# Kernel optimization log

Hardware: AMD Instinct MI355X
Metric: run time of the kernel (lower is better)

Reference implementation:

```python
import jax, jax.numpy as jnp
import numpy as np

WP = 1.0     # warp_penalty
TEMP = 0.01  # soft-min temperature
BIG = 1e7    # finite stand-in for +inf (exp(-BIG/TEMP) == 0 exactly in fp32)


def setup_inputs() -> dict:
    key = jax.random.key(0)
    k1, k2, k3, k4 = jax.random.split(key, 4)
    B, T1, T2, C = 8, 256, 1024, 128
    fea_a = jax.random.normal(k1, (B, T1, C), jnp.float32)
    fea_b = jax.random.normal(k2, (B, T2, C), jnp.float32)
    len_a = jax.random.randint(k3, (B,), T1 // 2, T1 + 1)
    len_b = jax.random.randint(k4, (B,), T2 // 2, T2 + 1)
    return {"fea_a": fea_a, "len_a": len_a, "fea_b": fea_b, "len_b": len_b}


def _softmin(v, temp):
    # v: [3, B, T1]; stable -temp*log(sum(exp(-v/temp)))
    m = jnp.min(v, axis=0)
    return m - temp * jnp.log(jnp.sum(jnp.exp(-(v - m) / temp), axis=0))


def _soft_dtw(fea_a, fea_b, len_a, len_b, wp=WP, temp=TEMP):
    B, T1, C = fea_a.shape
    T2 = fea_b.shape[1]
    # L1 cost: [B, T2, T1]  (rows index fea_b, cols index fea_a, as in torch code)
    cost = jnp.mean(jnp.abs(fea_a[:, None, :, :] - fea_b[:, :, None, :]), axis=-1)
    # skewed cost: skew[b, d, j] = cost[b, clip(d-j, 0, T2-1), j]
    D = T1 + T2 - 1
    d = jnp.arange(D)[:, None]
    j = jnp.arange(T1)[None, :]
    idx = jnp.clip(d - j, 0, T2 - 1)           # [D, T1]
    skew = cost[:, idx, j]                      # [B, D, T1]
    skew = jnp.swapaxes(skew, 0, 1)             # [D, B, T1] for scan

    pc0 = jnp.full((B, T1 + 1), BIG, jnp.float32)       # path_cost (diag d-1)
    pcp0 = pc0.at[:, 0].set(0.0)                         # path_cost_prev (diag d-2)

    def step(carry, crow):
        pc, pcp = carry
        dirs = jnp.stack([pcp[:, :-1], pc[:, 1:] + wp, pc[:, :-1] + wp], axis=0)
        new = crow + _softmin(dirs, temp)                # [B, T1]
        new = jnp.concatenate([jnp.full((B, 1), BIG, new.dtype), new], axis=1)
        return (new, pc), new

    _, ys = jax.lax.scan(step, (pc0, pcp0), skew)        # ys: [D, B, T1+1]
    # per-sample answer: diagonal len_a+len_b-2, entry len_a
    di = len_a + len_b - 2
    loss_i = ys[di, jnp.arange(B), len_a]
    return jnp.sum(loss_i)  # reduction='mean' over a length-1 accumulator == sum


def reference(fea_a, len_a, fea_b, len_b):
    return _soft_dtw(fea_a, fea_b, len_a, len_b)
```

## Files before the change

### kernel.cpp

```cpp
#include <hip/hip_runtime.h>
#include <hip/hip_bf16.h>
#include <cstddef>

#define BIGV 10000000.0f
#define WPV  1.0f

#define BATCH 8
#define T1N 256
#define T2N 1024
#define CN 128
#define DN 1279

#define RPB 16
#define NSLOT 3
#define SLOT_BYTES (RPB * 1024)

__global__ __launch_bounds__(256) void cost_kernel(const float* __restrict__ A,
                                                   const float* __restrict__ Bf,
                                                   const int* __restrict__ lenA,
                                                   const int* __restrict__ lenB,
                                                   float* __restrict__ sk) {
    __shared__ float As[64 * 64];
    __shared__ float Bs[127 * 64];

    const int b  = blockIdx.z;
    const int d0 = blockIdx.y * 64;
    const int j0 = blockIdx.x * 64;
    const int tid = threadIdx.x;

    const int dEnd = lenA[b] + lenB[b] - 2;
    if (d0 > dEnd) return;

    const float* Ab = A  + (size_t)b * T1N * CN;
    const float* Bb = Bf + (size_t)b * T2N * CN;

    const int tj = tid & 15;
    const int td = tid >> 4;
    const int brow0 = td - tj + 63;
    const int rbase = d0 - j0 - 63;

    float acc[4][4];
    #pragma unroll
    for (int i = 0; i < 4; ++i)
        #pragma unroll
        for (int j = 0; j < 4; ++j) acc[i][j] = 0.0f;

#define SW(row, cq) (((row) << 6) + ((((cq) + (row)) & 15) << 2))

    for (int h = 0; h < 2; ++h) {
        const int ch0 = h * 64;
        #pragma unroll
        for (int i = 0; i < 4; ++i) {
            int idx = tid + i * 256;
            int row = idx >> 4;
            int cq  = idx & 15;
            float4 f = *(const float4*)(Ab + (size_t)(j0 + row) * CN + ch0 + (cq << 2));
            *(float4*)&As[SW(row, cq)] = f;
        }
        #pragma unroll
        for (int i = 0; i < 8; ++i) {
            int idx = tid + i * 256;
            if (idx < 2032) {
                int row = idx >> 4;
                int cq  = idx & 15;
                int gr = rbase + row;
                gr = gr < 0 ? 0 : (gr > T2N - 1 ? T2N - 1 : gr);
                float4 f = *(const float4*)(Bb + (size_t)gr * CN + ch0 + (cq << 2));
                *(float4*)&Bs[SW(row, cq)] = f;
            }
        }
        __syncthreads();

        for (int cq = 0; cq < 16; ++cq) {
            float4 a4[4], bv[7];
            #pragma unroll
            for (int ji = 0; ji < 4; ++ji) {
                int row = tj + 16 * ji;
                a4[ji] = *(const float4*)&As[SW(row, cq)];
            }
            #pragma unroll
            for (int m = 0; m < 7; ++m) {
                int row = brow0 + 16 * (m - 3);
                bv[m] = *(const float4*)&Bs[SW(row, cq)];
            }
            #pragma unroll
            for (int dk = 0; dk < 4; ++dk) {
                #pragma unroll
                for (int ji = 0; ji < 4; ++ji) {
                    float4 aa = a4[ji];
                    float4 bb = bv[dk - ji + 3];
                    acc[dk][ji] += fabsf(aa.x - bb.x) + fabsf(aa.y - bb.y)
                                 + fabsf(aa.z - bb.z) + fabsf(aa.w - bb.w);
                }
            }
        }
        __syncthreads();
    }
#undef SW

    #pragma unroll
    for (int dk = 0; dk < 4; ++dk) {
        int d = d0 + td + 16 * dk;
        if (d < DN) {
            size_t rowoff = ((size_t)b * DN + d) * T1N;
            #pragma unroll
            for (int ji = 0; ji < 4; ++ji) {
                int j = j0 + tj + 16 * ji;
                sk[rowoff + j] = acc[dk][ji] * (1.0f / 128.0f);
            }
        }
    }
}

__global__ __launch_bounds__(128, 1) void dp_wave_kernel(const float* __restrict__ sk,
                                                         const int* __restrict__ lenA,
                                                         const int* __restrict__ lenB,
                                                         float* __restrict__ out) {
    __shared__ char ring[NSLOT * SLOT_BYTES];
    __shared__ int prod_cnt;
    __shared__ int cons_cnt;

    const int b = blockIdx.x;
    if (threadIdx.x == 0) { prod_cnt = 0; cons_cnt = 0; }
    __syncthreads();

    const int wave = threadIdx.x >> 6;
    const int L = threadIdx.x & 63;

    const int la = __builtin_amdgcn_readfirstlane(lenA[b]);
    const int lb = __builtin_amdgcn_readfirstlane(lenB[b]);
    const int dEnd = la + lb - 2;
    const int kLast = dEnd >> 4;
    const int nblk = kLast + 1;

    if (wave == 1) {
        const float* skbp = sk + (size_t)b * DN * T1N + (L << 2);
        for (int k = 0; k < nblk; ++k) {
            if (k >= NSLOT) {
                while (__hip_atomic_load(&cons_cnt, __ATOMIC_ACQUIRE,
                                         __HIP_MEMORY_SCOPE_WORKGROUP) < k - (NSLOT - 1))
                    __builtin_amdgcn_s_sleep(1);
            }
            char* slot = ring + (k % NSLOT) * SLOT_BYTES;
            const int r0 = k * RPB;
            #pragma unroll
            for (int r = 0; r < RPB; ++r) {
                int row = r0 + r; row = row > DN - 1 ? DN - 1 : row;
                __builtin_amdgcn_global_load_lds(
                    (const __attribute__((address_space(1))) void*)(skbp + (size_t)row * T1N),
                    (__attribute__((address_space(3))) void*)(slot + (r << 10)),
                    16, 0, 0);
            }
            asm volatile("s_waitcnt vmcnt(16)" ::: "memory");
            if (L == 0)
                __hip_atomic_store(&prod_cnt, k, __ATOMIC_RELEASE,
                                   __HIP_MEMORY_SCOPE_WORKGROUP);
        }
        asm volatile("s_waitcnt vmcnt(0)" ::: "memory");
        if (L == 0)
            __hip_atomic_store(&prod_cnt, nblk, __ATOMIC_RELEASE,
                               __HIP_MEMORY_SCOPE_WORKGROUP);
        return;
    }

    float v1_0 = BIGV, v1_1 = BIGV, v1_2 = BIGV, v1_3 = BIGV;
    float v2_0 = BIGV, v2_1 = BIGV, v2_2 = BIGV, v2_3 = BIGV;
    float p1_prev = (L == 0) ? 0.0f : BIGV;

#define SHFL_UP1(SRC)                                                       \
    __int_as_float(__builtin_amdgcn_update_dpp(                             \
        __float_as_int(BIGV), __float_as_int(SRC),                          \
        0x138 , 0xF, 0xF, false))

#define DP_STEP(C4) do {                                                    \
        float4 c = (C4);                                                    \
        float p1 = SHFL_UP1(v1_3);                                          \
        float p2 = p1_prev;                                                 \
        float n0 = c.x + fminf(p2,   fminf(v1_0, p1)   + WPV);              \
        float n1 = c.y + fminf(v2_0, fminf(v1_1, v1_0) + WPV);              \
        float n2 = c.z + fminf(v2_1, fminf(v1_2, v1_1) + WPV);              \
        float n3 = c.w + fminf(v2_2, fminf(v1_3, v1_2) + WPV);              \
        p1_prev = p1;                                                       \
        v2_0 = v1_0; v2_1 = v1_1; v2_2 = v1_2; v2_3 = v1_3;                 \
        v1_0 = n0;   v1_1 = n1;   v1_2 = n2;   v1_3 = n3;                   \
    } while (0)

#define DP_STEP_G(C4, R) do {                                               \
        float4 c = (C4);                                                    \
        float p1 = SHFL_UP1(v1_3);                                          \
        float p2 = p1_prev;                                                 \
        float n0 = c.x + fminf(p2,   fminf(v1_0, p1)   + WPV);              \
        float n1 = c.y + fminf(v2_0, fminf(v1_1, v1_0) + WPV);              \
        float n2 = c.z + fminf(v2_1, fminf(v1_2, v1_1) + WPV);              \
        float n3 = c.w + fminf(v2_2, fminf(v1_3, v1_2) + WPV);              \
        if ((R) <= rem) {                                                   \
            p1_prev = p1;                                                   \
            v2_0 = v1_0; v2_1 = v1_1; v2_2 = v1_2; v2_3 = v1_3;             \
            v1_0 = n0;   v1_1 = n1;   v1_2 = n2;   v1_3 = n3;               \
        }                                                                   \
    } while (0)

#define WAIT_BLK(K) do {                                                    \
        while (__hip_atomic_load(&prod_cnt, __ATOMIC_ACQUIRE,               \
                                 __HIP_MEMORY_SCOPE_WORKGROUP) < (K) + 1)   \
            __builtin_amdgcn_s_sleep(1);                                    \
    } while (0)

#define READ_BLK(K)                                                         \
        const char* slot = ring + ((K) % NSLOT) * SLOT_BYTES;               \
        const float4* rp = (const float4*)(slot + (L << 4));                \
        float4 c0  = rp[0 * 64],  c1  = rp[1 * 64],  c2  = rp[2 * 64],  c3  = rp[3 * 64];  \
        float4 c4_ = rp[4 * 64],  c5  = rp[5 * 64],  c6  = rp[6 * 64],  c7  = rp[7 * 64];  \
        float4 c8  = rp[8 * 64],  c9  = rp[9 * 64],  c10 = rp[10 * 64], c11 = rp[11 * 64]; \
        float4 c12 = rp[12 * 64], c13 = rp[13 * 64], c14 = rp[14 * 64], c15 = rp[15 * 64]; \
        __builtin_amdgcn_sched_barrier(0);

    for (int k = 0; k < kLast; ++k) {
        WAIT_BLK(k);
        READ_BLK(k);
        DP_STEP(c0);  DP_STEP(c1);  DP_STEP(c2);  DP_STEP(c3);
        DP_STEP(c4_); DP_STEP(c5);  DP_STEP(c6);  DP_STEP(c7);
        DP_STEP(c8);  DP_STEP(c9);  DP_STEP(c10); DP_STEP(c11);
        DP_STEP(c12); DP_STEP(c13); DP_STEP(c14); DP_STEP(c15);
        if (L == 0)
            __hip_atomic_store(&cons_cnt, k + 1, __ATOMIC_RELEASE,
                               __HIP_MEMORY_SCOPE_WORKGROUP);
    }

    {
        const int rem = dEnd & 15;
        WAIT_BLK(kLast);
        READ_BLK(kLast);
        DP_STEP_G(c0, 0);   DP_STEP_G(c1, 1);   DP_STEP_G(c2, 2);   DP_STEP_G(c3, 3);
        DP_STEP_G(c4_, 4);  DP_STEP_G(c5, 5);   DP_STEP_G(c6, 6);   DP_STEP_G(c7, 7);
        DP_STEP_G(c8, 8);   DP_STEP_G(c9, 9);   DP_STEP_G(c10, 10); DP_STEP_G(c11, 11);
        DP_STEP_G(c12, 12); DP_STEP_G(c13, 13); DP_STEP_G(c14, 14); DP_STEP_G(c15, 15);
    }

    const int tcap = la - 1;
    if (L == (tcap >> 2)) {
        const int k = tcap & 3;
        float r = v1_0;
        if (k == 1) r = v1_1;
        else if (k == 2) r = v1_2;
        else if (k == 3) r = v1_3;
        atomicAdd(out, r);
    }
#undef READ_BLK
#undef WAIT_BLK
#undef DP_STEP_G
#undef DP_STEP
#undef SHFL_UP1
}

extern "C" void kernel_launch(void* const* d_in, const int* in_sizes, int n_in,
                              void* d_out, int out_size, void* d_ws, size_t ws_size,
                              hipStream_t stream) {
    const float* feaA = (const float*)d_in[0];
    const int*   lenA = (const int*)d_in[1];
    const float* feaB = (const float*)d_in[2];
    const int*   lenB = (const int*)d_in[3];

    float* sk = (float*)d_ws;

    hipMemsetAsync(d_out, 0, sizeof(float), stream);
    cost_kernel<<<dim3(T1N / 64, (DN + 63) / 64, BATCH), 256, 0, stream>>>(feaA, feaB, lenA, lenB, sk);
    dp_wave_kernel<<<BATCH, 128, 0, stream>>>(sk, lenA, lenB, (float*)d_out);
}
```

Baseline: 160.3 us.

## Replace producer-wave ring with single-wave self-prefetched LDS pipeline

Removes the dedicated producer wave and the LDS atomic counters it used to hand blocks to the consumer. The DP wave now issues its own async global-to-LDS loads three blocks ahead into a four-slot ring and waits on vmcnt instead of spin-polling shared counters. This drops the sleep/poll handshake latency from the serial critical path, but the DMA issue now sits inside the consumer's loop. Correctness depends on in-order vmcnt accounting and on no slot being overwritten while it is still being read.

```diff
diff --git a/kernel.cpp b/kernel.cpp
--- a/kernel.cpp
+++ b/kernel.cpp
@@ -12,7 +12,7 @@
 #define DN 1279
 
 #define RPB 16
-#define NSLOT 3
+#define NSLOT 4
 #define SLOT_BYTES (RPB * 1024)
 
 __global__ __launch_bounds__(256) void cost_kernel(const float* __restrict__ A,
@@ -112,56 +112,34 @@
     }
 }
 
-__global__ __launch_bounds__(128, 1) void dp_wave_kernel(const float* __restrict__ sk,
-                                                         const int* __restrict__ lenA,
-                                                         const int* __restrict__ lenB,
-                                                         float* __restrict__ out) {
+__global__ __launch_bounds__(64, 1) void dp_wave_kernel(const float* __restrict__ sk,
+                                                        const int* __restrict__ lenA,
+                                                        const int* __restrict__ lenB,
+                                                        float* __restrict__ out) {
     __shared__ char ring[NSLOT * SLOT_BYTES];
-    __shared__ int prod_cnt;
-    __shared__ int cons_cnt;
 
     const int b = blockIdx.x;
-    if (threadIdx.x == 0) { prod_cnt = 0; cons_cnt = 0; }
-    __syncthreads();
-
-    const int wave = threadIdx.x >> 6;
-    const int L = threadIdx.x & 63;
+    const int L = threadIdx.x;
 
     const int la = __builtin_amdgcn_readfirstlane(lenA[b]);
     const int lb = __builtin_amdgcn_readfirstlane(lenB[b]);
     const int dEnd = la + lb - 2;
     const int kLast = dEnd >> 4;
-    const int nblk = kLast + 1;
-
-    if (wave == 1) {
-        const float* skbp = sk + (size_t)b * DN * T1N + (L << 2);
-        for (int k = 0; k < nblk; ++k) {
-            if (k >= NSLOT) {
-                while (__hip_atomic_load(&cons_cnt, __ATOMIC_ACQUIRE,
-                                         __HIP_MEMORY_SCOPE_WORKGROUP) < k - (NSLOT - 1))
-                    __builtin_amdgcn_s_sleep(1);
-            }
-            char* slot = ring + (k % NSLOT) * SLOT_BYTES;
-            const int r0 = k * RPB;
-            #pragma unroll
-            for (int r = 0; r < RPB; ++r) {
-                int row = r0 + r; row = row > DN - 1 ? DN - 1 : row;
-                __builtin_amdgcn_global_load_lds(
-                    (const __attribute__((address_space(1))) void*)(skbp + (size_t)row * T1N),
-                    (__attribute__((address_space(3))) void*)(slot + (r << 10)),
-                    16, 0, 0);
-            }
-            asm volatile("s_waitcnt vmcnt(16)" ::: "memory");
-            if (L == 0)
-                __hip_atomic_store(&prod_cnt, k, __ATOMIC_RELEASE,
-                                   __HIP_MEMORY_SCOPE_WORKGROUP);
-        }
-        asm volatile("s_waitcnt vmcnt(0)" ::: "memory");
-        if (L == 0)
-            __hip_atomic_store(&prod_cnt, nblk, __ATOMIC_RELEASE,
-                               __HIP_MEMORY_SCOPE_WORKGROUP);
-        return;
-    }
+
+    const float* skbp = sk + (size_t)b * DN * T1N + (L << 2);
+
+#define DMA_BLK(K) do {                                                     \
+        char* _slot = ring + ((K) & (NSLOT - 1)) * SLOT_BYTES;              \
+        const int _r0 = (K) * RPB;                                          \
+        _Pragma("unroll")                                                   \
+        for (int _r = 0; _r < RPB; ++_r) {                                  \
+            int _row = _r0 + _r; _row = _row > DN - 1 ? DN - 1 : _row;      \
+            __builtin_amdgcn_global_load_lds(                               \
+                (const __attribute__((address_space(1))) void*)(skbp + (size_t)_row * T1N), \
+                (__attribute__((address_space(3))) void*)(_slot + (_r << 10)), \
+                16, 0, 0);                                                  \
+        }                                                                   \
+    } while (0)
 
     float v1_0 = BIGV, v1_1 = BIGV, v1_2 = BIGV, v1_3 = BIGV;
     float v2_0 = BIGV, v2_1 = BIGV, v2_2 = BIGV, v2_3 = BIGV;
@@ -200,14 +178,10 @@
         }                                                                   \
     } while (0)
 
-#define WAIT_BLK(K) do {                                                    \
-        while (__hip_atomic_load(&prod_cnt, __ATOMIC_ACQUIRE,               \
-                                 __HIP_MEMORY_SCOPE_WORKGROUP) < (K) + 1)   \
-            __builtin_amdgcn_s_sleep(1);                                    \
-    } while (0)
+#define WAIT32() asm volatile("s_waitcnt vmcnt(32)" ::: "memory")
 
 #define READ_BLK(K)                                                         \
-        const char* slot = ring + ((K) % NSLOT) * SLOT_BYTES;               \
+        const char* slot = ring + ((K) & (NSLOT - 1)) * SLOT_BYTES;         \
         const float4* rp = (const float4*)(slot + (L << 4));                \
         float4 c0  = rp[0 * 64],  c1  = rp[1 * 64],  c2  = rp[2 * 64],  c3  = rp[3 * 64];  \
         float4 c4_ = rp[4 * 64],  c5  = rp[5 * 64],  c6  = rp[6 * 64],  c7  = rp[7 * 64];  \
@@ -215,27 +189,29 @@
         float4 c12 = rp[12 * 64], c13 = rp[13 * 64], c14 = rp[14 * 64], c15 = rp[15 * 64]; \
         __builtin_amdgcn_sched_barrier(0);
 
+    DMA_BLK(0); DMA_BLK(1); DMA_BLK(2);
+
     for (int k = 0; k < kLast; ++k) {
-        WAIT_BLK(k);
+        WAIT32();
         READ_BLK(k);
+        DMA_BLK(k + 3);
         DP_STEP(c0);  DP_STEP(c1);  DP_STEP(c2);  DP_STEP(c3);
         DP_STEP(c4_); DP_STEP(c5);  DP_STEP(c6);  DP_STEP(c7);
         DP_STEP(c8);  DP_STEP(c9);  DP_STEP(c10); DP_STEP(c11);
         DP_STEP(c12); DP_STEP(c13); DP_STEP(c14); DP_STEP(c15);
-        if (L == 0)
-            __hip_atomic_store(&cons_cnt, k + 1, __ATOMIC_RELEASE,
-                               __HIP_MEMORY_SCOPE_WORKGROUP);
     }
 
     {
         const int rem = dEnd & 15;
-        WAIT_BLK(kLast);
+        WAIT32();
         READ_BLK(kLast);
         DP_STEP_G(c0, 0);   DP_STEP_G(c1, 1);   DP_STEP_G(c2, 2);   DP_STEP_G(c3, 3);
         DP_STEP_G(c4_, 4);  DP_STEP_G(c5, 5);   DP_STEP_G(c6, 6);   DP_STEP_G(c7, 7);
         DP_STEP_G(c8, 8);   DP_STEP_G(c9, 9);   DP_STEP_G(c10, 10); DP_STEP_G(c11, 11);
         DP_STEP_G(c12, 12); DP_STEP_G(c13, 13); DP_STEP_G(c14, 14); DP_STEP_G(c15, 15);
     }
+
+    asm volatile("s_waitcnt vmcnt(0)" ::: "memory");
 
     const int tcap = la - 1;
     if (L == (tcap >> 2)) {
@@ -247,10 +223,11 @@
         atomicAdd(out, r);
     }
 #undef READ_BLK
-#undef WAIT_BLK
+#undef WAIT32
 #undef DP_STEP_G
 #undef DP_STEP
 #undef SHFL_UP1
+#undef DMA_BLK
 }
 
 extern "C" void kernel_launch(void* const* d_in, const int* in_sizes, int n_in,
@@ -265,5 +242,5 @@
 
     hipMemsetAsync(d_out, 0, sizeof(float), stream);
     cost_kernel<<<dim3(T1N / 64, (DN + 63) / 64, BATCH), 256, 0, stream>>>(feaA, feaB, lenA, lenB, sk);
-    dp_wave_kernel<<<BATCH, 128, 0, stream>>>(sk, lenA, lenB, (float*)d_out);
+    dp_wave_kernel<<<BATCH, 64, 0, stream>>>(sk, lenA, lenB, (float*)d_out);
 }
```

Result: slower. 189.4 us (+18.2%).

## Fuse cost and DP kernels into one persistent launch with tile-ready counters

Applied to the files above, without the earlier changes.

Merges the cost-matrix kernel and the wavefront DP kernel into a single launch. Eight blocks run the DP while 256 worker blocks compute cost tiles in diagonal-major order and bump per-(batch, diagonal-band) global counters. The DP producer wave polls these counters before streaming rows, so the DP can start before the whole cost matrix exists. Wave priorities are also raised for the DP waves. The risks are correctness depending on the DP blocks and workers being co-resident, extra memset and atomic traffic, and DP blocks stalling on slow tiles.

```diff
diff --git a/kernel.cpp b/kernel.cpp
--- a/kernel.cpp
+++ b/kernel.cpp
@@ -10,122 +10,145 @@
 #define T2N 1024
 #define CN 128
 #define DN 1279
+#define NDT 20
+#define NTILE 640
+#define NWORK 256
 
 #define RPB 16
 #define NSLOT 3
 #define SLOT_BYTES (RPB * 1024)
-
-__global__ __launch_bounds__(256) void cost_kernel(const float* __restrict__ A,
-                                                   const float* __restrict__ Bf,
-                                                   const int* __restrict__ lenA,
-                                                   const int* __restrict__ lenB,
-                                                   float* __restrict__ sk) {
-    __shared__ float As[64 * 64];
-    __shared__ float Bs[127 * 64];
-
-    const int b  = blockIdx.z;
-    const int d0 = blockIdx.y * 64;
-    const int j0 = blockIdx.x * 64;
-    const int tid = threadIdx.x;
-
-    const int dEnd = lenA[b] + lenB[b] - 2;
-    if (d0 > dEnd) return;
-
-    const float* Ab = A  + (size_t)b * T1N * CN;
-    const float* Bb = Bf + (size_t)b * T2N * CN;
-
-    const int tj = tid & 15;
-    const int td = tid >> 4;
-    const int brow0 = td - tj + 63;
-    const int rbase = d0 - j0 - 63;
-
-    float acc[4][4];
-    #pragma unroll
-    for (int i = 0; i < 4; ++i)
-        #pragma unroll
-        for (int j = 0; j < 4; ++j) acc[i][j] = 0.0f;
+#define LDS_BYTES 49216
+
+__global__ __launch_bounds__(256, 1) void fused_kernel(const float* __restrict__ A,
+                                                       const float* __restrict__ Bf,
+                                                       const int* __restrict__ lenA,
+                                                       const int* __restrict__ lenB,
+                                                       float* __restrict__ sk,
+                                                       int* __restrict__ cnt,
+                                                       float* __restrict__ out) {
+    __shared__ __align__(16) char lds[LDS_BYTES];
+
+    const int bid = blockIdx.x;
+
+    if (bid >= BATCH) {
+        float* As = (float*)lds;
+        float* Bs = (float*)(lds + 16384);
+        const int tid = threadIdx.x;
+        const int tj = tid & 15;
+        const int td = tid >> 4;
 
 #define SW(row, cq) (((row) << 6) + ((((cq) + (row)) & 15) << 2))
 
-    for (int h = 0; h < 2; ++h) {
-        const int ch0 = h * 64;
-        #pragma unroll
-        for (int i = 0; i < 4; ++i) {
-            int idx = tid + i * 256;
-            int row = idx >> 4;
-            int cq  = idx & 15;
-            float4 f = *(const float4*)(Ab + (size_t)(j0 + row) * CN + ch0 + (cq << 2));
-            *(float4*)&As[SW(row, cq)] = f;
-        }
-        #pragma unroll
-        for (int i = 0; i < 8; ++i) {
-            int idx = tid + i * 256;
-            if (idx < 2032) {
-                int row = idx >> 4;
-                int cq  = idx & 15;
-                int gr = rbase + row;
-                gr = gr < 0 ? 0 : (gr > T2N - 1 ? T2N - 1 : gr);
-                float4 f = *(const float4*)(Bb + (size_t)gr * CN + ch0 + (cq << 2));
-                *(float4*)&Bs[SW(row, cq)] = f;
-            }
-        }
-        __syncthreads();
-
-        for (int cq = 0; cq < 16; ++cq) {
-            float4 a4[4], bv[7];
+        for (int t = bid - BATCH; t < NTILE; t += NWORK) {
+            const int y  = t >> 5;
+            const int b  = (t >> 2) & 7;
+            const int jb = t & 3;
+            const int d0 = y * 64;
+            const int j0 = jb * 64;
+
+            const int dEnd = lenA[b] + lenB[b] - 2;
+            if (d0 > dEnd) {
+                if (tid == 0)
+                    __hip_atomic_fetch_add(&cnt[b * NDT + y], 1,
+                                           __ATOMIC_RELEASE, __HIP_MEMORY_SCOPE_AGENT);
+                continue;
+            }
+
+            const float* Ab = A  + (size_t)b * T1N * CN;
+            const float* Bb = Bf + (size_t)b * T2N * CN;
+            const int brow0 = td - tj + 63;
+            const int rbase = d0 - j0 - 63;
+
+            float acc[4][4];
             #pragma unroll
-            for (int ji = 0; ji < 4; ++ji) {
-                int row = tj + 16 * ji;
-                a4[ji] = *(const float4*)&As[SW(row, cq)];
-            }
-            #pragma unroll
-            for (int m = 0; m < 7; ++m) {
-                int row = brow0 + 16 * (m - 3);
-                bv[m] = *(const float4*)&Bs[SW(row, cq)];
-            }
+            for (int i = 0; i < 4; ++i)
+                #pragma unroll
+                for (int j = 0; j < 4; ++j) acc[i][j] = 0.0f;
+
+            for (int h = 0; h < 2; ++h) {
+                const int ch0 = h * 64;
+                #pragma unroll
+                for (int i = 0; i < 4; ++i) {
+                    int idx = tid + i * 256;
+                    int row = idx >> 4;
+                    int cq  = idx & 15;
+                    float4 f = *(const float4*)(Ab + (size_t)(j0 + row) * CN + ch0 + (cq << 2));
+                    *(float4*)&As[SW(row, cq)] = f;
+                }
+                #pragma unroll
+                for (int i = 0; i < 8; ++i) {
+                    int idx = tid + i * 256;
+                    if (idx < 2032) {
+                        int row = idx >> 4;
+                        int cq  = idx & 15;
+                        int gr = rbase + row;
+                        gr = gr < 0 ? 0 : (gr > T2N - 1 ? T2N - 1 : gr);
+                        float4 f = *(const float4*)(Bb + (size_t)gr * CN + ch0 + (cq << 2));
+                        *(float4*)&Bs[SW(row, cq)] = f;
+                    }
+                }
+                __syncthreads();
+
+                for (int cq = 0; cq < 16; ++cq) {
+                    float4 a4[4], bv[7];
+                    #pragma unroll
+                    for (int ji = 0; ji < 4; ++ji) {
+                        int row = tj + 16 * ji;
+                        a4[ji] = *(const float4*)&As[SW(row, cq)];
+                    }
+                    #pragma unroll
+                    for (int m = 0; m < 7; ++m) {
+                        int row = brow0 + 16 * (m - 3);
+                        bv[m] = *(const float4*)&Bs[SW(row, cq)];
+                    }
+                    #pragma unroll
+                    for (int dk = 0; dk < 4; ++dk) {
+                        #pragma unroll
+                        for (int ji = 0; ji < 4; ++ji) {
+                            float4 aa = a4[ji];
+                            float4 bb = bv[dk - ji + 3];
+                            acc[dk][ji] += fabsf(aa.x - bb.x) + fabsf(aa.y - bb.y)
+                                         + fabsf(aa.z - bb.z) + fabsf(aa.w - bb.w);
+                        }
+                    }
+                }
+                __syncthreads();
+            }
+
             #pragma unroll
             for (int dk = 0; dk < 4; ++dk) {
-                #pragma unroll
-                for (int ji = 0; ji < 4; ++ji) {
-                    float4 aa = a4[ji];
-                    float4 bb = bv[dk - ji + 3];
-                    acc[dk][ji] += fabsf(aa.x - bb.x) + fabsf(aa.y - bb.y)
-                                 + fabsf(aa.z - bb.z) + fabsf(aa.w - bb.w);
+                int d = d0 + td + 16 * dk;
+                if (d < DN) {
+                    size_t rowoff = ((size_t)b * DN + d) * T1N;
+                    #pragma unroll
+                    for (int ji = 0; ji < 4; ++ji) {
+                        int j = j0 + tj + 16 * ji;
+                        sk[rowoff + j] = acc[dk][ji] * (1.0f / 128.0f);
+                    }
                 }
             }
+
+            __threadfence();
+            __syncthreads();
+            if (tid == 0)
+                __hip_atomic_fetch_add(&cnt[b * NDT + y], 1,
+                                       __ATOMIC_RELEASE, __HIP_MEMORY_SCOPE_AGENT);
         }
-        __syncthreads();
-    }
 #undef SW
-
-    #pragma unroll
-    for (int dk = 0; dk < 4; ++dk) {
-        int d = d0 + td + 16 * dk;
-        if (d < DN) {
-            size_t rowoff = ((size_t)b * DN + d) * T1N;
-            #pragma unroll
-            for (int ji = 0; ji < 4; ++ji) {
-                int j = j0 + tj + 16 * ji;
-                sk[rowoff + j] = acc[dk][ji] * (1.0f / 128.0f);
-            }
-        }
-    }
-}
-
-__global__ __launch_bounds__(128, 1) void dp_wave_kernel(const float* __restrict__ sk,
-                                                         const int* __restrict__ lenA,
-                                                         const int* __restrict__ lenB,
-                                                         float* __restrict__ out) {
-    __shared__ char ring[NSLOT * SLOT_BYTES];
-    __shared__ int prod_cnt;
-    __shared__ int cons_cnt;
-
-    const int b = blockIdx.x;
-    if (threadIdx.x == 0) { prod_cnt = 0; cons_cnt = 0; }
+        return;
+    }
+
+    char* ring = lds;
+    int* prod_cnt = (int*)(lds + NSLOT * SLOT_BYTES);
+    int* cons_cnt = prod_cnt + 1;
+
+    const int b = bid;
+    if (threadIdx.x == 0) { *prod_cnt = 0; *cons_cnt = 0; }
     __syncthreads();
 
     const int wave = threadIdx.x >> 6;
     const int L = threadIdx.x & 63;
+    if (wave >= 2) return;
 
     const int la = __builtin_amdgcn_readfirstlane(lenA[b]);
     const int lb = __builtin_amdgcn_readfirstlane(lenB[b]);
@@ -134,10 +157,20 @@
     const int nblk = kLast + 1;
 
     if (wave == 1) {
+        asm volatile("s_setprio 1");
+        const int* cntb = cnt + b * NDT;
         const float* skbp = sk + (size_t)b * DN * T1N + (L << 2);
+        int y_ck = 0;
         for (int k = 0; k < nblk; ++k) {
+            int ygate = k * 16 + 15; if (ygate > dEnd) ygate = dEnd;
+            ygate >>= 6;
+            while (y_ck <= ygate) {
+                if (__hip_atomic_load(&cntb[y_ck], __ATOMIC_ACQUIRE,
+                                      __HIP_MEMORY_SCOPE_AGENT) == 4) ++y_ck;
+                else __builtin_amdgcn_s_sleep(2);
+            }
             if (k >= NSLOT) {
-                while (__hip_atomic_load(&cons_cnt, __ATOMIC_ACQUIRE,
+                while (__hip_atomic_load(cons_cnt, __ATOMIC_ACQUIRE,
                                          __HIP_MEMORY_SCOPE_WORKGROUP) < k - (NSLOT - 1))
                     __builtin_amdgcn_s_sleep(1);
             }
@@ -153,15 +186,17 @@
             }
             asm volatile("s_waitcnt vmcnt(16)" ::: "memory");
             if (L == 0)
-                __hip_atomic_store(&prod_cnt, k, __ATOMIC_RELEASE,
+                __hip_atomic_store(prod_cnt, k, __ATOMIC_RELEASE,
                                    __HIP_MEMORY_SCOPE_WORKGROUP);
         }
         asm volatile("s_waitcnt vmcnt(0)" ::: "memory");
         if (L == 0)
-            __hip_atomic_store(&prod_cnt, nblk, __ATOMIC_RELEASE,
+            __hip_atomic_store(prod_cnt, nblk, __ATOMIC_RELEASE,
                                __HIP_MEMORY_SCOPE_WORKGROUP);
         return;
     }
+
+    asm volatile("s_setprio 2");
 
     float v1_0 = BIGV, v1_1 = BIGV, v1_2 = BIGV, v1_3 = BIGV;
     float v2_0 = BIGV, v2_1 = BIGV, v2_2 = BIGV, v2_3 = BIGV;
@@ -201,7 +236,7 @@
     } while (0)
 
 #define WAIT_BLK(K) do {                                                    \
-        while (__hip_atomic_load(&prod_cnt, __ATOMIC_ACQUIRE,               \
+        while (__hip_atomic_load(prod_cnt, __ATOMIC_ACQUIRE,                \
                                  __HIP_MEMORY_SCOPE_WORKGROUP) < (K) + 1)   \
             __builtin_amdgcn_s_sleep(1);                                    \
     } while (0)
@@ -223,7 +258,7 @@
         DP_STEP(c8);  DP_STEP(c9);  DP_STEP(c10); DP_STEP(c11);
         DP_STEP(c12); DP_STEP(c13); DP_STEP(c14); DP_STEP(c15);
         if (L == 0)
-            __hip_atomic_store(&cons_cnt, k + 1, __ATOMIC_RELEASE,
+            __hip_atomic_store(cons_cnt, k + 1, __ATOMIC_RELEASE,
                                __HIP_MEMORY_SCOPE_WORKGROUP);
     }
 
@@ -262,8 +297,10 @@
     const int*   lenB = (const int*)d_in[3];
 
     float* sk = (float*)d_ws;
-
+    int* cnt = (int*)((char*)d_ws + (size_t)BATCH * DN * T1N * sizeof(float));
+
+    hipMemsetAsync(cnt, 0, BATCH * NDT * sizeof(int), stream);
     hipMemsetAsync(d_out, 0, sizeof(float), stream);
-    cost_kernel<<<dim3(T1N / 64, (DN + 63) / 64, BATCH), 256, 0, stream>>>(feaA, feaB, lenA, lenB, sk);
-    dp_wave_kernel<<<BATCH, 128, 0, stream>>>(sk, lenA, lenB, (float*)d_out);
+    fused_kernel<<<BATCH + NWORK, 256, 0, stream>>>(feaA, feaB, lenA, lenB,
+                                                    sk, cnt, (float*)d_out);
 }
```

New measurement: 197.4 us. 1.23x slower.
